# Optimization experiments

Hardware: AMD Instinct MI355X
Metric: run time of the kernel (lower is better)

The kernel has to match this reference:

```python
import jax, jax.numpy as jnp
import numpy as np


def setup_inputs() -> dict:
    key = jax.random.key(0)
    k1, k2, k3 = jax.random.split(key, 3)
    B, H, W = 32, 512, 512
    N = H * W  # tokens
    K = 32768  # positive_trials
    decision_scores = jax.random.normal(k1, (B, N, 2), dtype=jnp.float32)
    s_map = jax.random.uniform(k2, (B, 1, H, W), dtype=jnp.float32)
    # uniform noise for gumbel sampling, kept away from {0,1} for log stability
    u = jax.random.uniform(k3, (B, N, 2), dtype=jnp.float32, minval=1e-6, maxval=1.0 - 1e-6)
    return {"decision_scores": decision_scores, "s_map": s_map, "u": u, "positive_trials": K}


def reference(decision_scores, s_map, u, positive_trials):
    B, N, _ = decision_scores.shape
    # gumbel_softmax(hard=False, tau=1): softmax(logits + gumbel_noise)
    gumbel = -jnp.log(-jnp.log(u))
    logp = jax.nn.log_softmax(decision_scores + gumbel, axis=-1)  # [B, N, 2]
    # soft_decisions = p[..., 0]
    # Tokenizer: [B, 1, H, W] -> [B, N, 1]; use channel 0 as salience score.
    scores = s_map.reshape(B, 1, -1).transpose(0, 2, 1)[..., 0]  # [B, N]
    # argsort descending, take top-k indices == lax.top_k indices
    _, idx = jax.lax.top_k(scores, positive_trials)  # [B, K]
    trials = jnp.zeros((B, N), dtype=decision_scores.dtype)
    trials = trials.at[jnp.arange(B)[:, None], idx].set(1.0)  # scatter ones
    # BCE(sum): -sum(t*log(p) + (1-t)*log(1-p)); with 2-class softmax, 1-p0 = p1.
    # torch BCE clamps log terms at -100.
    logp0 = jnp.clip(logp[..., 0], -100.0)
    logp1 = jnp.clip(logp[..., 1], -100.0)
    loss = -jnp.sum(trials * logp0 + (1.0 - trials) * logp1)
    return loss
```

## Files before the change

kernel.cpp:

```cpp
#include <hip/hip_runtime.h>

#define NB    4096
#define CAP   4096
#define BATCH 32
#define NTOK  262144
#define LOSS_BLOCKS 8192

__device__ __forceinline__ int bucket_of(float v) {
    int b = (int)(v * (float)NB);
    return b > NB - 1 ? NB - 1 : b;
}

__global__ void hist_kernel(const float* __restrict__ smap, int* __restrict__ hist) {
    __shared__ int lh[NB];
    for (int i = threadIdx.x; i < NB; i += blockDim.x) lh[i] = 0;
    __syncthreads();
    const int cbpb = 8;
    int b  = blockIdx.x / cbpb;
    int cb = blockIdx.x % cbpb;
    const int chunk = NTOK / cbpb;
    const float4* src = (const float4*)(smap + (size_t)b * NTOK + (size_t)cb * chunk);
    const int nf4 = chunk / 4;
    for (int i = threadIdx.x; i < nf4; i += blockDim.x) {
        float4 v = src[i];
        atomicAdd(&lh[bucket_of(v.x)], 1);
        atomicAdd(&lh[bucket_of(v.y)], 1);
        atomicAdd(&lh[bucket_of(v.z)], 1);
        atomicAdd(&lh[bucket_of(v.w)], 1);
    }
    __syncthreads();
    int* gh = hist + b * NB;
    for (int i = threadIdx.x; i < NB; i += blockDim.x) {
        int c = lh[i];
        if (c) atomicAdd(&gh[i], c);
    }
}

__global__ void select_kernel(const int* __restrict__ hist, const int* __restrict__ kptr,
                              int* __restrict__ tbR) {
    int b = blockIdx.x;
    const int* gh = hist + b * NB;
    __shared__ int h[NB];
    __shared__ int csum[256];
    __shared__ int above[256];
    int t = threadIdx.x;
    const int C = NB / 256;
    int base = t * C;
    int s = 0;
    for (int i = 0; i < C; i++) { int v = gh[base + i]; h[base + i] = v; s += v; }
    csum[t] = s;
    __syncthreads();
    if (t == 0) {
        int acc = 0;
        for (int c = 255; c >= 0; c--) { above[c] = acc; acc += csum[c]; }
    }
    __syncthreads();
    int K = *kptr;
    int cum = above[t];
    for (int i = C - 1; i >= 0; i--) {
        int hb = h[base + i];
        if (cum < K && cum + hb >= K) {
            tbR[2 * b]     = base + i;
            tbR[2 * b + 1] = K - cum;
        }
        cum += hb;
    }
}

__global__ void collect_kernel(const float* __restrict__ smap, const int* __restrict__ tbR,
                               int* __restrict__ cnt, float* __restrict__ cval,
                               int* __restrict__ cidx) {
    const int cbpb = 64;
    int b  = blockIdx.x / cbpb;
    int cb = blockIdx.x % cbpb;
    const int chunk = NTOK / cbpb;
    int tb = tbR[2 * b];
    const float4* src = (const float4*)(smap + (size_t)b * NTOK + (size_t)cb * chunk);
    const int nf4 = chunk / 4;
    int base_n = cb * chunk;
    for (int i = threadIdx.x; i < nf4; i += blockDim.x) {
        float4 v = src[i];
        float vals[4] = {v.x, v.y, v.z, v.w};
#pragma unroll
        for (int s = 0; s < 4; s++) {
            if (bucket_of(vals[s]) == tb) {
                int p = atomicAdd(&cnt[b], 1);
                if (p < CAP) {
                    cval[b * CAP + p] = vals[s];
                    cidx[b * CAP + p] = base_n + 4 * i + s;
                }
            }
        }
    }
}

__global__ void refine_kernel(const int* __restrict__ tbR, const int* __restrict__ cnt,
                              const float* __restrict__ cval, const int* __restrict__ cidx,
                              float* __restrict__ T, int* __restrict__ ncut) {
    int b = blockIdx.x;
    int R = tbR[2 * b + 1];
    int M = cnt[b];
    bool overflow = (M > CAP);
    if (M > CAP) M = CAP;
    __shared__ float sv[CAP];
    __shared__ int   si[CAP];
    for (int i = threadIdx.x; i < M; i += blockDim.x) {
        sv[i] = cval[b * CAP + i];
        si[i] = cidx[b * CAP + i];
    }
    __syncthreads();
    if (overflow || R > M || R < 1) {
        if (threadIdx.x == 0) { T[b] = (float)tbR[2 * b] / (float)NB; ncut[b] = 0x7fffffff; }
        return;
    }
    for (int i = threadIdx.x; i < M; i += blockDim.x) {
        float vi = sv[i]; int ii = si[i];
        int r = 0;
        for (int j = 0; j < M; j++) {
            float vj = sv[j];
            r += (vj > vi) || (vj == vi && si[j] < ii);
        }
        if (r == R - 1) { T[b] = vi; ncut[b] = ii; }
    }
}

__device__ __forceinline__ float token_loss(float d0, float d1, float u0, float u1,
                                            bool sel) {
    float g0 = -__logf(-__logf(u0));
    float g1 = -__logf(-__logf(u1));
    float dd = (d0 + g0) - (d1 + g1);
    float l  = __logf(1.f + __expf(-fabsf(dd)));
    float lp0 = (dd >= 0.f) ? -l      : dd - l;
    float lp1 = (dd >= 0.f) ? -l - dd : -l;
    lp0 = fmaxf(lp0, -100.f); lp1 = fmaxf(lp1, -100.f);
    return sel ? -lp0 : -lp1;
}

__global__ void loss_kernel(const float* __restrict__ ds, const float* __restrict__ u,
                            const float* __restrict__ smap, const float* __restrict__ T,
                            const int* __restrict__ ncut, float* __restrict__ partials) {
    int tid = blockIdx.x * blockDim.x + threadIdx.x;
    int b = tid >> 16;
    int p = tid & 65535;
    const float4* ds4 = (const float4*)(ds + (size_t)b * NTOK * 2);
    const float4* u4  = (const float4*)(u  + (size_t)b * NTOK * 2);
    const float4* s4  = (const float4*)(smap + (size_t)b * NTOK);
    float4 dA = ds4[2 * p];
    float4 dB = ds4[2 * p + 1];
    float4 uA = u4[2 * p];
    float4 uB = u4[2 * p + 1];
    float4 sv = s4[p];
    float Tb = T[b];
    int   nc = ncut[b];
    int   n0 = p << 2;

    bool s0 = (sv.x > Tb) || (sv.x == Tb && (n0 + 0) <= nc);
    bool s1 = (sv.y > Tb) || (sv.y == Tb && (n0 + 1) <= nc);
    bool s2 = (sv.z > Tb) || (sv.z == Tb && (n0 + 2) <= nc);
    bool s3 = (sv.w > Tb) || (sv.w == Tb && (n0 + 3) <= nc);

    float acc = token_loss(dA.x, dA.y, uA.x, uA.y, s0)
              + token_loss(dA.z, dA.w, uA.z, uA.w, s1)
              + token_loss(dB.x, dB.y, uB.x, uB.y, s2)
              + token_loss(dB.z, dB.w, uB.z, uB.w, s3);

    for (int off = 32; off > 0; off >>= 1) acc += __shfl_down(acc, off, 64);
    __shared__ float red[4];
    int lane = threadIdx.x & 63, wv = threadIdx.x >> 6;
    if (lane == 0) red[wv] = acc;
    __syncthreads();
    if (threadIdx.x == 0)
        partials[blockIdx.x] = red[0] + red[1] + red[2] + red[3];
}

__global__ void reduce_kernel(const float* __restrict__ partials, float* __restrict__ out) {
    float acc = 0.f;
    for (int i = threadIdx.x; i < LOSS_BLOCKS; i += blockDim.x) acc += partials[i];
    for (int off = 32; off > 0; off >>= 1) acc += __shfl_down(acc, off, 64);
    __shared__ float red[16];
    int lane = threadIdx.x & 63, wv = threadIdx.x >> 6;
    if (lane == 0) red[wv] = acc;
    __syncthreads();
    if (threadIdx.x == 0) {
        float s = 0.f;
        for (int w = 0; w < (int)(blockDim.x >> 6); w++) s += red[w];
        out[0] = s;
    }
}

extern "C" void kernel_launch(void* const* d_in, const int* in_sizes, int n_in,
                              void* d_out, int out_size, void* d_ws, size_t ws_size,
                              hipStream_t stream) {
    const float* ds   = (const float*)d_in[0];
    const float* smap = (const float*)d_in[1];
    const float* u    = (const float*)d_in[2];
    const int*   kptr = (const int*)d_in[3];

    int*   hist = (int*)d_ws;
    int*   cnt  = hist + BATCH * NB;
    int*   tbR  = cnt + BATCH;
    float* T    = (float*)(tbR + 2 * BATCH);
    int*   ncut = (int*)(T + BATCH);
    float* cval = (float*)(ncut + BATCH);
    int*   cidx = (int*)(cval + BATCH * CAP);
    float* partials = (float*)(cidx + BATCH * CAP);

    hipMemsetAsync(hist, 0, (size_t)(BATCH * NB + BATCH) * sizeof(int), stream);

    hist_kernel<<<256, 1024, 0, stream>>>(smap, hist);
    select_kernel<<<BATCH, 256, 0, stream>>>(hist, kptr, tbR);
    collect_kernel<<<2048, 256, 0, stream>>>(smap, tbR, cnt, cval, cidx);
    refine_kernel<<<BATCH, 256, 0, stream>>>(tbR, cnt, cval, cidx, T, ncut);
    loss_kernel<<<LOSS_BLOCKS, 256, 0, stream>>>(ds, u, smap, T, ncut, partials);
    reduce_kernel<<<1, 1024, 0, stream>>>(partials, (float*)d_out);
}
```

Baseline: 210.3 us.

## Fuse top-k selection and loss pipeline into one cooperative persistent kernel

```diff
diff --git a/kernel.cpp b/kernel.cpp
--- a/kernel.cpp
+++ b/kernel.cpp
@@ -1,127 +1,20 @@
 #include <hip/hip_runtime.h>
-
-#define NB    4096
-#define CAP   4096
+#include <hip/hip_cooperative_groups.h>
+
+namespace cg = cooperative_groups;
+
+#define NB2   2048
+#define CAP2  2048
 #define BATCH 32
 #define NTOK  262144
-#define LOSS_BLOCKS 8192
-
-__device__ __forceinline__ int bucket_of(float v) {
-    int b = (int)(v * (float)NB);
-    return b > NB - 1 ? NB - 1 : b;
-}
-
-__global__ void hist_kernel(const float* __restrict__ smap, int* __restrict__ hist) {
-    __shared__ int lh[NB];
-    for (int i = threadIdx.x; i < NB; i += blockDim.x) lh[i] = 0;
-    __syncthreads();
-    const int cbpb = 8;
-    int b  = blockIdx.x / cbpb;
-    int cb = blockIdx.x % cbpb;
-    const int chunk = NTOK / cbpb;
-    const float4* src = (const float4*)(smap + (size_t)b * NTOK + (size_t)cb * chunk);
-    const int nf4 = chunk / 4;
-    for (int i = threadIdx.x; i < nf4; i += blockDim.x) {
-        float4 v = src[i];
-        atomicAdd(&lh[bucket_of(v.x)], 1);
-        atomicAdd(&lh[bucket_of(v.y)], 1);
-        atomicAdd(&lh[bucket_of(v.z)], 1);
-        atomicAdd(&lh[bucket_of(v.w)], 1);
-    }
-    __syncthreads();
-    int* gh = hist + b * NB;
-    for (int i = threadIdx.x; i < NB; i += blockDim.x) {
-        int c = lh[i];
-        if (c) atomicAdd(&gh[i], c);
-    }
-}
-
-__global__ void select_kernel(const int* __restrict__ hist, const int* __restrict__ kptr,
-                              int* __restrict__ tbR) {
-    int b = blockIdx.x;
-    const int* gh = hist + b * NB;
-    __shared__ int h[NB];
-    __shared__ int csum[256];
-    __shared__ int above[256];
-    int t = threadIdx.x;
-    const int C = NB / 256;
-    int base = t * C;
-    int s = 0;
-    for (int i = 0; i < C; i++) { int v = gh[base + i]; h[base + i] = v; s += v; }
-    csum[t] = s;
-    __syncthreads();
-    if (t == 0) {
-        int acc = 0;
-        for (int c = 255; c >= 0; c--) { above[c] = acc; acc += csum[c]; }
-    }
-    __syncthreads();
-    int K = *kptr;
-    int cum = above[t];
-    for (int i = C - 1; i >= 0; i--) {
-        int hb = h[base + i];
-        if (cum < K && cum + hb >= K) {
-            tbR[2 * b]     = base + i;
-            tbR[2 * b + 1] = K - cum;
-        }
-        cum += hb;
-    }
-}
-
-__global__ void collect_kernel(const float* __restrict__ smap, const int* __restrict__ tbR,
-                               int* __restrict__ cnt, float* __restrict__ cval,
-                               int* __restrict__ cidx) {
-    const int cbpb = 64;
-    int b  = blockIdx.x / cbpb;
-    int cb = blockIdx.x % cbpb;
-    const int chunk = NTOK / cbpb;
-    int tb = tbR[2 * b];
-    const float4* src = (const float4*)(smap + (size_t)b * NTOK + (size_t)cb * chunk);
-    const int nf4 = chunk / 4;
-    int base_n = cb * chunk;
-    for (int i = threadIdx.x; i < nf4; i += blockDim.x) {
-        float4 v = src[i];
-        float vals[4] = {v.x, v.y, v.z, v.w};
-#pragma unroll
-        for (int s = 0; s < 4; s++) {
-            if (bucket_of(vals[s]) == tb) {
-                int p = atomicAdd(&cnt[b], 1);
-                if (p < CAP) {
-                    cval[b * CAP + p] = vals[s];
-                    cidx[b * CAP + p] = base_n + 4 * i + s;
-                }
-            }
-        }
-    }
-}
-
-__global__ void refine_kernel(const int* __restrict__ tbR, const int* __restrict__ cnt,
-                              const float* __restrict__ cval, const int* __restrict__ cidx,
-                              float* __restrict__ T, int* __restrict__ ncut) {
-    int b = blockIdx.x;
-    int R = tbR[2 * b + 1];
-    int M = cnt[b];
-    bool overflow = (M > CAP);
-    if (M > CAP) M = CAP;
-    __shared__ float sv[CAP];
-    __shared__ int   si[CAP];
-    for (int i = threadIdx.x; i < M; i += blockDim.x) {
-        sv[i] = cval[b * CAP + i];
-        si[i] = cidx[b * CAP + i];
-    }
-    __syncthreads();
-    if (overflow || R > M || R < 1) {
-        if (threadIdx.x == 0) { T[b] = (float)tbR[2 * b] / (float)NB; ncut[b] = 0x7fffffff; }
-        return;
-    }
-    for (int i = threadIdx.x; i < M; i += blockDim.x) {
-        float vi = sv[i]; int ii = si[i];
-        int r = 0;
-        for (int j = 0; j < M; j++) {
-            float vj = sv[j];
-            r += (vj > vi) || (vj == vi && si[j] < ii);
-        }
-        if (r == R - 1) { T[b] = vi; ncut[b] = ii; }
-    }
+#define GRID  1024
+#define BLOCK 256
+#define BPB   32
+#define SLICE 8192
+
+__device__ __forceinline__ int bucket2(float v) {
+    int b = (int)(v * (float)NB2);
+    return b > NB2 - 1 ? NB2 - 1 : b;
 }
 
 __device__ __forceinline__ float token_loss(float d0, float d1, float u0, float u1,
@@ -136,55 +29,168 @@
     return sel ? -lp0 : -lp1;
 }
 
-__global__ void loss_kernel(const float* __restrict__ ds, const float* __restrict__ u,
-                            const float* __restrict__ smap, const float* __restrict__ T,
-                            const int* __restrict__ ncut, float* __restrict__ partials) {
-    int tid = blockIdx.x * blockDim.x + threadIdx.x;
-    int b = tid >> 16;
-    int p = tid & 65535;
-    const float4* ds4 = (const float4*)(ds + (size_t)b * NTOK * 2);
-    const float4* u4  = (const float4*)(u  + (size_t)b * NTOK * 2);
-    const float4* s4  = (const float4*)(smap + (size_t)b * NTOK);
-    float4 dA = ds4[2 * p];
-    float4 dB = ds4[2 * p + 1];
-    float4 uA = u4[2 * p];
-    float4 uB = u4[2 * p + 1];
-    float4 sv = s4[p];
-    float Tb = T[b];
-    int   nc = ncut[b];
-    int   n0 = p << 2;
-
-    bool s0 = (sv.x > Tb) || (sv.x == Tb && (n0 + 0) <= nc);
-    bool s1 = (sv.y > Tb) || (sv.y == Tb && (n0 + 1) <= nc);
-    bool s2 = (sv.z > Tb) || (sv.z == Tb && (n0 + 2) <= nc);
-    bool s3 = (sv.w > Tb) || (sv.w == Tb && (n0 + 3) <= nc);
-
-    float acc = token_loss(dA.x, dA.y, uA.x, uA.y, s0)
-              + token_loss(dA.z, dA.w, uA.z, uA.w, s1)
-              + token_loss(dB.x, dB.y, uB.x, uB.y, s2)
-              + token_loss(dB.z, dB.w, uB.z, uB.w, s3);
-
-    for (int off = 32; off > 0; off >>= 1) acc += __shfl_down(acc, off, 64);
+__global__ __launch_bounds__(BLOCK, 8) void mega_kernel(
+        const float* __restrict__ ds, const float* __restrict__ smap,
+        const float* __restrict__ u, const int* __restrict__ kptr,
+        int* __restrict__ hist,
+        int* __restrict__ tbR,
+        float* __restrict__ T, int* __restrict__ ncut,
+        float* __restrict__ cval, int* __restrict__ cidx,
+        float* __restrict__ partials,
+        float* __restrict__ out) {
+    cg::grid_group grid = cg::this_grid();
+    __shared__ int smem[4096];
     __shared__ float red[4];
-    int lane = threadIdx.x & 63, wv = threadIdx.x >> 6;
-    if (lane == 0) red[wv] = acc;
+    const int tid = threadIdx.x;
+    const int blk = blockIdx.x;
+    const int b   = blk >> 5;
+    const int cb  = blk & 31;
+    int* cnt = hist + BATCH * NB2;
+
+    {
+        const int total = BATCH * NB2 + BATCH;
+        for (int i = blk * BLOCK + tid; i < total; i += GRID * BLOCK) hist[i] = 0;
+    }
+    int* lh = smem;
+    for (int i = tid; i < NB2; i += BLOCK) lh[i] = 0;
     __syncthreads();
-    if (threadIdx.x == 0)
-        partials[blockIdx.x] = red[0] + red[1] + red[2] + red[3];
-}
-
-__global__ void reduce_kernel(const float* __restrict__ partials, float* __restrict__ out) {
-    float acc = 0.f;
-    for (int i = threadIdx.x; i < LOSS_BLOCKS; i += blockDim.x) acc += partials[i];
-    for (int off = 32; off > 0; off >>= 1) acc += __shfl_down(acc, off, 64);
-    __shared__ float red[16];
-    int lane = threadIdx.x & 63, wv = threadIdx.x >> 6;
-    if (lane == 0) red[wv] = acc;
+    const float4* src = (const float4*)(smap + (size_t)b * NTOK + (size_t)cb * SLICE);
+    for (int i = tid; i < SLICE / 4; i += BLOCK) {
+        float4 v = src[i];
+        atomicAdd(&lh[bucket2(v.x)], 1);
+        atomicAdd(&lh[bucket2(v.y)], 1);
+        atomicAdd(&lh[bucket2(v.z)], 1);
+        atomicAdd(&lh[bucket2(v.w)], 1);
+    }
     __syncthreads();
-    if (threadIdx.x == 0) {
-        float s = 0.f;
-        for (int w = 0; w < (int)(blockDim.x >> 6); w++) s += red[w];
-        out[0] = s;
+    grid.sync();
+
+    {
+        int* gh = hist + b * NB2;
+        for (int i = tid; i < NB2; i += BLOCK) {
+            int c = lh[i];
+            if (c) atomicAdd(&gh[i], c);
+        }
+    }
+    grid.sync();
+
+    if (cb == 0) {
+        int* h     = smem;
+        int* csum  = smem + NB2;
+        int* above = smem + NB2 + 256;
+        const int C = NB2 / BLOCK;
+        const int* gh = hist + b * NB2;
+        int base = tid * C;
+        int s = 0;
+        for (int i = 0; i < C; i++) { int v = gh[base + i]; h[base + i] = v; s += v; }
+        csum[tid] = s;
+        __syncthreads();
+        if (tid == 0) {
+            int acc = 0;
+            for (int c = BLOCK - 1; c >= 0; c--) { above[c] = acc; acc += csum[c]; }
+        }
+        __syncthreads();
+        int K = *kptr;
+        int cum = above[tid];
+        for (int i = C - 1; i >= 0; i--) {
+            int hb = h[base + i];
+            if (cum < K && cum + hb >= K) {
+                tbR[2 * b]     = base + i;
+                tbR[2 * b + 1] = K - cum;
+            }
+            cum += hb;
+        }
+    }
+    grid.sync();
+
+    {
+        int tb = tbR[2 * b];
+        int base_n = cb * SLICE;
+        for (int i = tid; i < SLICE / 4; i += BLOCK) {
+            float4 v = src[i];
+            float vals[4] = {v.x, v.y, v.z, v.w};
+#pragma unroll
+            for (int s = 0; s < 4; s++) {
+                if (bucket2(vals[s]) == tb) {
+                    int p = atomicAdd(&cnt[b], 1);
+                    if (p < CAP2) {
+                        cval[b * CAP2 + p] = vals[s];
+                        cidx[b * CAP2 + p] = base_n + 4 * i + s;
+                    }
+                }
+            }
+        }
+    }
+    grid.sync();
+
+    if (cb == 0) {
+        int R = tbR[2 * b + 1];
+        int M = cnt[b];
+        bool ovf = (M > CAP2);
+        if (M > CAP2) M = CAP2;
+        float* sv = (float*)smem;
+        int*   si = smem + CAP2;
+        for (int i = tid; i < M; i += BLOCK) {
+            sv[i] = cval[b * CAP2 + i];
+            si[i] = cidx[b * CAP2 + i];
+        }
+        __syncthreads();
+        if (ovf || R > M || R < 1) {
+            if (tid == 0) { T[b] = (float)tbR[2 * b] / (float)NB2; ncut[b] = 0x7fffffff; }
+        } else {
+            for (int i = tid; i < M; i += BLOCK) {
+                float vi = sv[i]; int ii = si[i];
+                int r = 0;
+                for (int j = 0; j < M; j++) {
+                    float vj = sv[j];
+                    r += (vj > vi) || (vj == vi && si[j] < ii);
+                }
+                if (r == R - 1) { T[b] = vi; ncut[b] = ii; }
+            }
+        }
+    }
+    grid.sync();
+
+    {
+        float Tb = T[b];
+        int   nc = ncut[b];
+        const float4* ds4 = (const float4*)(ds + (size_t)b * NTOK * 2);
+        const float4* u4  = (const float4*)(u  + (size_t)b * NTOK * 2);
+        const float4* s4  = (const float4*)(smap + (size_t)b * NTOK);
+        float acc = 0.f;
+        for (int it = 0; it < 8; it++) {
+            int p = cb * (SLICE / 4) + it * BLOCK + tid;
+            float4 dA = ds4[2 * p];
+            float4 dB = ds4[2 * p + 1];
+            float4 uA = u4[2 * p];
+            float4 uB = u4[2 * p + 1];
+            float4 sv4 = s4[p];
+            int n0 = p << 2;
+            bool s0 = (sv4.x > Tb) || (sv4.x == Tb && (n0 + 0) <= nc);
+            bool s1 = (sv4.y > Tb) || (sv4.y == Tb && (n0 + 1) <= nc);
+            bool s2 = (sv4.z > Tb) || (sv4.z == Tb && (n0 + 2) <= nc);
+            bool s3 = (sv4.w > Tb) || (sv4.w == Tb && (n0 + 3) <= nc);
+            acc += token_loss(dA.x, dA.y, uA.x, uA.y, s0)
+                 + token_loss(dA.z, dA.w, uA.z, uA.w, s1)
+                 + token_loss(dB.x, dB.y, uB.x, uB.y, s2)
+                 + token_loss(dB.z, dB.w, uB.z, uB.w, s3);
+        }
+        for (int off = 32; off > 0; off >>= 1) acc += __shfl_down(acc, off, 64);
+        int lane = tid & 63, wv = tid >> 6;
+        if (lane == 0) red[wv] = acc;
+        __syncthreads();
+        if (tid == 0) partials[blk] = red[0] + red[1] + red[2] + red[3];
+    }
+    grid.sync();
+
+    if (blk == 0) {
+        float acc = 0.f;
+        for (int i = tid; i < GRID; i += BLOCK) acc += partials[i];
+        for (int off = 32; off > 0; off >>= 1) acc += __shfl_down(acc, off, 64);
+        int lane = tid & 63, wv = tid >> 6;
+        if (lane == 0) red[wv] = acc;
+        __syncthreads();
+        if (tid == 0) out[0] = red[0] + red[1] + red[2] + red[3];
     }
 }
 
@@ -197,20 +203,17 @@
     const int*   kptr = (const int*)d_in[3];
 
     int*   hist = (int*)d_ws;
-    int*   cnt  = hist + BATCH * NB;
-    int*   tbR  = cnt + BATCH;
+    int*   tbR  = hist + BATCH * NB2 + BATCH;
     float* T    = (float*)(tbR + 2 * BATCH);
     int*   ncut = (int*)(T + BATCH);
     float* cval = (float*)(ncut + BATCH);
-    int*   cidx = (int*)(cval + BATCH * CAP);
-    float* partials = (float*)(cidx + BATCH * CAP);
-
-    hipMemsetAsync(hist, 0, (size_t)(BATCH * NB + BATCH) * sizeof(int), stream);
-
-    hist_kernel<<<256, 1024, 0, stream>>>(smap, hist);
-    select_kernel<<<BATCH, 256, 0, stream>>>(hist, kptr, tbR);
-    collect_kernel<<<2048, 256, 0, stream>>>(smap, tbR, cnt, cval, cidx);
-    refine_kernel<<<BATCH, 256, 0, stream>>>(tbR, cnt, cval, cidx, T, ncut);
-    loss_kernel<<<LOSS_BLOCKS, 256, 0, stream>>>(ds, u, smap, T, ncut, partials);
-    reduce_kernel<<<1, 1024, 0, stream>>>(partials, (float*)d_out);
-}
+    int*   cidx = (int*)(cval + BATCH * CAP2);
+    float* partials = (float*)(cidx + BATCH * CAP2);
+    float* out = (float*)d_out;
+
+    void* args[] = {(void*)&ds, (void*)&smap, (void*)&u, (void*)&kptr,
+                    (void*)&hist, (void*)&tbR, (void*)&T, (void*)&ncut,
+                    (void*)&cval, (void*)&cidx, (void*)&partials, (void*)&out};
+    hipLaunchCooperativeKernel((void*)mega_kernel, dim3(GRID), dim3(BLOCK),
+                               args, 0, stream);
+}
```

Result: slower. 809.3 us (+284.7%).

## Fuse histogram, select, collect and refine into one per-batch prep kernel

Applied to the files above, without the earlier changes.

```diff
diff --git a/kernel.cpp b/kernel.cpp
--- a/kernel.cpp
+++ b/kernel.cpp
@@ -1,119 +1,90 @@
 #include <hip/hip_runtime.h>
 
 #define NB    4096
-#define CAP   4096
+#define CAP   1024
 #define BATCH 32
 #define NTOK  262144
-#define LOSS_BLOCKS 8192
+#define PT    1024
+#define LOSS_BLOCKS 4096
 
 __device__ __forceinline__ int bucket_of(float v) {
     int b = (int)(v * (float)NB);
     return b > NB - 1 ? NB - 1 : b;
 }
 
-__global__ void hist_kernel(const float* __restrict__ smap, int* __restrict__ hist) {
-    __shared__ int lh[NB];
-    for (int i = threadIdx.x; i < NB; i += blockDim.x) lh[i] = 0;
+__global__ __launch_bounds__(PT) void prep_kernel(const float* __restrict__ smap,
+                                                  const int* __restrict__ kptr,
+                                                  float* __restrict__ T,
+                                                  int* __restrict__ ncut) {
+    __shared__ int   hist[NB];
+    __shared__ int   sA[PT];
+    __shared__ int   sB[PT];
+    __shared__ float sv[CAP];
+    __shared__ int   si[CAP];
+    __shared__ int   cnt_s, tb_s, R_s;
+
+    const int tid = threadIdx.x;
+    const int b   = blockIdx.x;
+
+    for (int i = tid; i < NB; i += PT) hist[i] = 0;
+    if (tid == 0) cnt_s = 0;
     __syncthreads();
-    const int cbpb = 8;
-    int b  = blockIdx.x / cbpb;
-    int cb = blockIdx.x % cbpb;
-    const int chunk = NTOK / cbpb;
-    const float4* src = (const float4*)(smap + (size_t)b * NTOK + (size_t)cb * chunk);
-    const int nf4 = chunk / 4;
-    for (int i = threadIdx.x; i < nf4; i += blockDim.x) {
+
+    const float4* src = (const float4*)(smap + (size_t)b * NTOK);
+    const int NF4 = NTOK / 4;
+    for (int i = tid; i < NF4; i += PT) {
         float4 v = src[i];
-        atomicAdd(&lh[bucket_of(v.x)], 1);
-        atomicAdd(&lh[bucket_of(v.y)], 1);
-        atomicAdd(&lh[bucket_of(v.z)], 1);
-        atomicAdd(&lh[bucket_of(v.w)], 1);
+        atomicAdd(&hist[bucket_of(v.x)], 1);
+        atomicAdd(&hist[bucket_of(v.y)], 1);
+        atomicAdd(&hist[bucket_of(v.z)], 1);
+        atomicAdd(&hist[bucket_of(v.w)], 1);
     }
     __syncthreads();
-    int* gh = hist + b * NB;
-    for (int i = threadIdx.x; i < NB; i += blockDim.x) {
-        int c = lh[i];
-        if (c) atomicAdd(&gh[i], c);
+
+    const int C = NB / PT;
+    int base = tid * C;
+    int csum = hist[base] + hist[base + 1] + hist[base + 2] + hist[base + 3];
+    sA[tid] = csum;
+    __syncthreads();
+
+    int* pin = sA; int* pout = sB;
+    for (int st = 1; st < PT; st <<= 1) {
+        int v = pin[tid] + ((tid + st < PT) ? pin[tid + st] : 0);
+        pout[tid] = v;
+        __syncthreads();
+        int* t_ = pin; pin = pout; pout = t_;
     }
-}
+    int above = (tid < PT - 1) ? pin[tid + 1] : 0;
 
-__global__ void select_kernel(const int* __restrict__ hist, const int* __restrict__ kptr,
-                              int* __restrict__ tbR) {
-    int b = blockIdx.x;
-    const int* gh = hist + b * NB;
-    __shared__ int h[NB];
-    __shared__ int csum[256];
-    __shared__ int above[256];
-    int t = threadIdx.x;
-    const int C = NB / 256;
-    int base = t * C;
-    int s = 0;
-    for (int i = 0; i < C; i++) { int v = gh[base + i]; h[base + i] = v; s += v; }
-    csum[t] = s;
-    __syncthreads();
-    if (t == 0) {
-        int acc = 0;
-        for (int c = 255; c >= 0; c--) { above[c] = acc; acc += csum[c]; }
+    const int K = *kptr;
+    int cum = above;
+    for (int i = C - 1; i >= 0; i--) {
+        int hb = hist[base + i];
+        if (cum < K && cum + hb >= K) { tb_s = base + i; R_s = K - cum; }
+        cum += hb;
     }
     __syncthreads();
-    int K = *kptr;
-    int cum = above[t];
-    for (int i = C - 1; i >= 0; i--) {
-        int hb = h[base + i];
-        if (cum < K && cum + hb >= K) {
-            tbR[2 * b]     = base + i;
-            tbR[2 * b + 1] = K - cum;
-        }
-        cum += hb;
-    }
-}
+    const int tb = tb_s, R = R_s;
 
-__global__ void collect_kernel(const float* __restrict__ smap, const int* __restrict__ tbR,
-                               int* __restrict__ cnt, float* __restrict__ cval,
-                               int* __restrict__ cidx) {
-    const int cbpb = 64;
-    int b  = blockIdx.x / cbpb;
-    int cb = blockIdx.x % cbpb;
-    const int chunk = NTOK / cbpb;
-    int tb = tbR[2 * b];
-    const float4* src = (const float4*)(smap + (size_t)b * NTOK + (size_t)cb * chunk);
-    const int nf4 = chunk / 4;
-    int base_n = cb * chunk;
-    for (int i = threadIdx.x; i < nf4; i += blockDim.x) {
+    for (int i = tid; i < NF4; i += PT) {
         float4 v = src[i];
         float vals[4] = {v.x, v.y, v.z, v.w};
 #pragma unroll
-        for (int s = 0; s < 4; s++) {
-            if (bucket_of(vals[s]) == tb) {
-                int p = atomicAdd(&cnt[b], 1);
-                if (p < CAP) {
-                    cval[b * CAP + p] = vals[s];
-                    cidx[b * CAP + p] = base_n + 4 * i + s;
-                }
+        for (int c = 0; c < 4; c++) {
+            if (bucket_of(vals[c]) == tb) {
+                int p = atomicAdd(&cnt_s, 1);
+                if (p < CAP) { sv[p] = vals[c]; si[p] = 4 * i + c; }
             }
         }
     }
-}
+    __syncthreads();
 
-__global__ void refine_kernel(const int* __restrict__ tbR, const int* __restrict__ cnt,
-                              const float* __restrict__ cval, const int* __restrict__ cidx,
-                              float* __restrict__ T, int* __restrict__ ncut) {
-    int b = blockIdx.x;
-    int R = tbR[2 * b + 1];
-    int M = cnt[b];
-    bool overflow = (M > CAP);
-    if (M > CAP) M = CAP;
-    __shared__ float sv[CAP];
-    __shared__ int   si[CAP];
-    for (int i = threadIdx.x; i < M; i += blockDim.x) {
-        sv[i] = cval[b * CAP + i];
-        si[i] = cidx[b * CAP + i];
-    }
-    __syncthreads();
-    if (overflow || R > M || R < 1) {
-        if (threadIdx.x == 0) { T[b] = (float)tbR[2 * b] / (float)NB; ncut[b] = 0x7fffffff; }
+    int M = cnt_s;
+    if (M > CAP || R > M || R < 1) {
+        if (tid == 0) { T[b] = (float)tb / (float)NB; ncut[b] = 0x7fffffff; }
         return;
     }
-    for (int i = threadIdx.x; i < M; i += blockDim.x) {
+    for (int i = tid; i < M; i += PT) {
         float vi = sv[i]; int ii = si[i];
         int r = 0;
         for (int j = 0; j < M; j++) {
@@ -140,29 +111,44 @@
                             const float* __restrict__ smap, const float* __restrict__ T,
                             const int* __restrict__ ncut, float* __restrict__ partials) {
     int tid = blockIdx.x * blockDim.x + threadIdx.x;
-    int b = tid >> 16;
-    int p = tid & 65535;
+    int b  = tid >> 15;
+    int p8 = tid & 32767;
     const float4* ds4 = (const float4*)(ds + (size_t)b * NTOK * 2);
     const float4* u4  = (const float4*)(u  + (size_t)b * NTOK * 2);
     const float4* s4  = (const float4*)(smap + (size_t)b * NTOK);
-    float4 dA = ds4[2 * p];
-    float4 dB = ds4[2 * p + 1];
-    float4 uA = u4[2 * p];
-    float4 uB = u4[2 * p + 1];
-    float4 sv = s4[p];
+
+    float4 d0 = ds4[4 * p8 + 0];
+    float4 d1 = ds4[4 * p8 + 1];
+    float4 d2 = ds4[4 * p8 + 2];
+    float4 d3 = ds4[4 * p8 + 3];
+    float4 u0 = u4[4 * p8 + 0];
+    float4 u1 = u4[4 * p8 + 1];
+    float4 u2 = u4[4 * p8 + 2];
+    float4 u3 = u4[4 * p8 + 3];
+    float4 sa = s4[2 * p8 + 0];
+    float4 sb = s4[2 * p8 + 1];
+
     float Tb = T[b];
     int   nc = ncut[b];
-    int   n0 = p << 2;
+    int   n0 = p8 << 3;
 
-    bool s0 = (sv.x > Tb) || (sv.x == Tb && (n0 + 0) <= nc);
-    bool s1 = (sv.y > Tb) || (sv.y == Tb && (n0 + 1) <= nc);
-    bool s2 = (sv.z > Tb) || (sv.z == Tb && (n0 + 2) <= nc);
-    bool s3 = (sv.w > Tb) || (sv.w == Tb && (n0 + 3) <= nc);
+    bool e0 = (sa.x > Tb) || (sa.x == Tb && (n0 + 0) <= nc);
+    bool e1 = (sa.y > Tb) || (sa.y == Tb && (n0 + 1) <= nc);
+    bool e2 = (sa.z > Tb) || (sa.z == Tb && (n0 + 2) <= nc);
+    bool e3 = (sa.w > Tb) || (sa.w == Tb && (n0 + 3) <= nc);
+    bool e4 = (sb.x > Tb) || (sb.x == Tb && (n0 + 4) <= nc);
+    bool e5 = (sb.y > Tb) || (sb.y == Tb && (n0 + 5) <= nc);
+    bool e6 = (sb.z > Tb) || (sb.z == Tb && (n0 + 6) <= nc);
+    bool e7 = (sb.w > Tb) || (sb.w == Tb && (n0 + 7) <= nc);
 
-    float acc = token_loss(dA.x, dA.y, uA.x, uA.y, s0)
-              + token_loss(dA.z, dA.w, uA.z, uA.w, s1)
-              + token_loss(dB.x, dB.y, uB.x, uB.y, s2)
-              + token_loss(dB.z, dB.w, uB.z, uB.w, s3);
+    float acc = token_loss(d0.x, d0.y, u0.x, u0.y, e0)
+              + token_loss(d0.z, d0.w, u0.z, u0.w, e1)
+              + token_loss(d1.x, d1.y, u1.x, u1.y, e2)
+              + token_loss(d1.z, d1.w, u1.z, u1.w, e3)
+              + token_loss(d2.x, d2.y, u2.x, u2.y, e4)
+              + token_loss(d2.z, d2.w, u2.z, u2.w, e5)
+              + token_loss(d3.x, d3.y, u3.x, u3.y, e6)
+              + token_loss(d3.z, d3.w, u3.z, u3.w, e7);
 
     for (int off = 32; off > 0; off >>= 1) acc += __shfl_down(acc, off, 64);
     __shared__ float red[4];
@@ -196,21 +182,11 @@
     const float* u    = (const float*)d_in[2];
     const int*   kptr = (const int*)d_in[3];
 
-    int*   hist = (int*)d_ws;
-    int*   cnt  = hist + BATCH * NB;
-    int*   tbR  = cnt + BATCH;
-    float* T    = (float*)(tbR + 2 * BATCH);
+    float* T    = (float*)d_ws;
     int*   ncut = (int*)(T + BATCH);
-    float* cval = (float*)(ncut + BATCH);
-    int*   cidx = (int*)(cval + BATCH * CAP);
-    float* partials = (float*)(cidx + BATCH * CAP);
+    float* partials = (float*)(ncut + BATCH);
 
-    hipMemsetAsync(hist, 0, (size_t)(BATCH * NB + BATCH) * sizeof(int), stream);
-
-    hist_kernel<<<256, 1024, 0, stream>>>(smap, hist);
-    select_kernel<<<BATCH, 256, 0, stream>>>(hist, kptr, tbR);
-    collect_kernel<<<2048, 256, 0, stream>>>(smap, tbR, cnt, cval, cidx);
-    refine_kernel<<<BATCH, 256, 0, stream>>>(tbR, cnt, cval, cidx, T, ncut);
+    prep_kernel<<<BATCH, PT, 0, stream>>>(smap, kptr, T, ncut);
     loss_kernel<<<LOSS_BLOCKS, 256, 0, stream>>>(ds, u, smap, T, ncut, partials);
     reduce_kernel<<<1, 1024, 0, stream>>>(partials, (float*)d_out);
 }
```

New measurement: 233.9 us. +11.2%, slower.
